# Optimization experiments

Measured on AMD Instinct MI355X. Metric: run time of the kernel, lower is better.

The kernel has to match this reference:

```python
import math
import jax, jax.numpy as jnp
import numpy as np

B, L, D, H = 2, 2048, 1024, 16
DH = D // H

def setup_inputs() -> dict:
    key = jax.random.key(0)
    ks = jax.random.split(key, 8)
    def xavier(k, fan_in, fan_out, shape):
        lim = math.sqrt(6.0 / (fan_in + fan_out))
        return jax.random.uniform(k, shape, jnp.float32, -lim, lim)
    x = jax.random.normal(ks[0], (B, L, D), jnp.float32)
    mask = jnp.ones((B, L), jnp.int32)
    # weights stored (in, out) so y = x @ W + b (equivalent to torch Linear)
    W_qkv = xavier(ks[1], D, 3 * D, (D, 3 * D))
    b_qkv = jnp.zeros((3 * D,), jnp.float32)
    W_out = xavier(ks[2], D, D, (D, D))
    b_out = jnp.zeros((D,), jnp.float32)
    W_phase = xavier(ks[3], D, H, (D, H))
    b_phase = jax.random.normal(ks[4], (H,), jnp.float32) * 0.02
    resonance_scale = jnp.float32(0.1)
    phase_scale = jnp.float32(1.0)
    return {"x": x, "mask": mask, "W_qkv": W_qkv, "b_qkv": b_qkv,
            "W_out": W_out, "b_out": b_out, "W_phase": W_phase,
            "b_phase": b_phase, "resonance_scale": resonance_scale,
            "phase_scale": phase_scale}

def reference(x, mask, W_qkv, b_qkv, W_out, b_out, W_phase, b_phase,
              resonance_scale, phase_scale):
    # qkv: (B,L,3D) -> (3,B,H,L,dh)
    qkv = (x @ W_qkv + b_qkv).reshape(B, L, 3, H, DH).transpose(2, 0, 3, 1, 4)
    q, k, v = qkv[0], qkv[1], qkv[2]
    scores = jnp.einsum('bhqd,bhkd->bhqk', q, k) / math.sqrt(DH)
    # per-token per-head phase (B,H,L)
    phase_val = jnp.tanh(phase_scale * (x @ W_phase + b_phase)).transpose(0, 2, 1)
    phase_diff = (phase_val[:, :, :, None] - phase_val[:, :, None, :]) ** 2
    scores = scores - resonance_scale * phase_diff
    # mask: (B,L) -> (B,1,1,L)
    m = mask[:, None, None, :]
    scores = jnp.where(m == 0, jnp.float32(-1e9), scores)
    attn = jax.nn.softmax(scores, axis=-1)
    out = jnp.einsum('bhqk,bhkd->bhqd', attn, v)  # (B,H,L,dh)
    out = out.transpose(0, 2, 1, 3).reshape(B, L, D)
    return out @ W_out + b_out
```

## Files before the change

kernel.cpp:

```cpp
#include <hip/hip_runtime.h>

typedef unsigned short u16;
typedef unsigned int u32;
typedef unsigned long long u64;
typedef __attribute__((ext_vector_type(2))) unsigned long long u64x2;
typedef __attribute__((ext_vector_type(4))) unsigned short u16x4;
typedef __attribute__((ext_vector_type(8))) __bf16 bf16x8;
typedef __attribute__((ext_vector_type(4))) float f32x4;
typedef __attribute__((ext_vector_type(2))) float f32x2;

#define DEV static __device__ __forceinline__
#define LOG2E 1.4426950408889634f

DEV u16 f2bf(float f) { __bf16 h = (__bf16)f; return __builtin_bit_cast(u16, h); }

#define BB   2
#define LLEN 2048
#define DDIM 1024
#define HH   16
#define DH   64
#define MTOT 4096
#define N3   3072

DEV void gl16(const void* g, void* l) {
  __builtin_amdgcn_global_load_lds(
      (const __attribute__((address_space(1))) void*)g,
      (__attribute__((address_space(3))) void*)l, 16, 0, 0);
}
DEV void gl4(const void* g, void* l) {
  __builtin_amdgcn_global_load_lds(
      (const __attribute__((address_space(1))) void*)g,
      (__attribute__((address_space(3))) void*)l, 4, 0, 0);
}

DEV void stage64(const u16* org, size_t gsb, u16* lds, int lane, int wid) {
#pragma unroll
  for (int j = 0; j < 2; j++) {
    int inst = wid * 2 + j;
    int r8 = lane >> 3;
    int row = inst * 8 + r8;
    int s = (r8 & 3) | ((inst & 1) << 2);
    const char* src = (const char*)org + (size_t)row * gsb +
                      (((lane & 7) ^ s) << 4);
    gl16(src, (char*)lds + inst * 1024);
  }
}
DEV bf16x8 read128s(const u16* tile, int row, int colb) {
  return *reinterpret_cast<const bf16x8*>(
      (const char*)tile + row * 128 +
      (colb ^ (((row & 3) | (((row >> 3) & 1) << 2)) << 4)));
}

DEV void stage128x32(const u16* org, size_t gsb, u16* lds, int lane, int wid) {
#pragma unroll
  for (int j = 0; j < 2; j++) {
    int inst = wid + j * 4;
    int r16 = lane >> 2;
    const char* src = (const char*)org + (size_t)(inst * 16 + r16) * gsb +
                      ((((lane & 3) ^ (r16 & 3))) << 4);
    gl16(src, (char*)lds + inst * 1024);
  }
}
DEV bf16x8 read64(const u16* tile, int row, int colb) {
  return *reinterpret_cast<const bf16x8*>(
      (const char*)tile + row * 64 + (colb ^ ((row & 3) << 4)));
}

__global__ __launch_bounds__(256) void k_transpose_w(const float* __restrict__ W,
                                                     u16* __restrict__ WT,
                                                     int K, int N) {
  __shared__ float s[32][33];
  int k0 = blockIdx.x * 32, n0 = blockIdx.y * 32;
  int tx = threadIdx.x & 31, ty = threadIdx.x >> 5;
#pragma unroll
  for (int i = 0; i < 4; i++)
    s[ty + i * 8][tx] = W[(k0 + ty + i * 8) * (size_t)N + n0 + tx];
  __syncthreads();
#pragma unroll
  for (int i = 0; i < 4; i++)
    WT[(size_t)(n0 + ty + i * 8) * K + k0 + tx] = f2bf(s[tx][ty + i * 8]);
}

__global__ __launch_bounds__(256) void k_phase(const float* __restrict__ x,
                                               const float* __restrict__ Wp,
                                               const float* __restrict__ bp,
                                               const float* __restrict__ pscale,
                                               const float* __restrict__ rscale,
                                               const int* __restrict__ mask,
                                               f32x2* __restrict__ ppk,
                                               u16* __restrict__ x_bf) {
  int m = blockIdx.x;
  int t = threadIdx.x;
  const float* xr = x + (size_t)m * DDIM;
  u16* xbr = x_bf + (size_t)m * DDIM;
  {
    f32x4 xv = *reinterpret_cast<const f32x4*>(xr + t * 4);
    u16x4 o;
    o.x = f2bf(xv.x); o.y = f2bf(xv.y); o.z = f2bf(xv.z); o.w = f2bf(xv.w);
    *reinterpret_cast<u16x4*>(xbr + t * 4) = o;
  }
  int h = t & 15, j = t >> 4;
  const float* wpb = Wp + h;
  float acc = 0.f;
#pragma unroll 4
  for (int kk4 = 0; kk4 < 16; kk4++) {
    int k0 = j * 64 + kk4 * 4;
    f32x4 xv = *reinterpret_cast<const f32x4*>(xr + k0);
    acc = fmaf(xv.x, wpb[(k0 + 0) * HH], acc);
    acc = fmaf(xv.y, wpb[(k0 + 1) * HH], acc);
    acc = fmaf(xv.z, wpb[(k0 + 2) * HH], acc);
    acc = fmaf(xv.w, wpb[(k0 + 3) * HH], acc);
  }
  __shared__ float s[16][17];
  s[j][h] = acc;
  __syncthreads();
  if (t < 16) {
    float sum = 0.f;
#pragma unroll
    for (int jj = 0; jj < 16; jj++) sum += s[jj][t];
    float v = tanhf((*pscale) * (sum + bp[t]));
    int b = m >> 11, l = m & (LLEN - 1);
    float kb = (mask[m] == 0) ? -1.0e9f : (-(*rscale) * LOG2E) * v * v;
    f32x2 o; o.x = v; o.y = kb;
    ppk[((size_t)(b * HH + t)) * LLEN + l] = o;
  }
}

template <bool BF16_OUT, bool QKV>
__global__ __launch_bounds__(256) void k_gemm(const u16* __restrict__ A,
                                              const u16* __restrict__ BT,
                                              const float* __restrict__ bias,
                                              void* __restrict__ C,
                                              u16* __restrict__ vT,
                                              int M, int N, int K) {
  __shared__ __attribute__((aligned(16))) u16 sS[4][128 * 32];
  int m0 = blockIdx.x * 128, n0 = blockIdx.y * 128;
  int t = threadIdx.x, lane = t & 63, wid = t >> 6;
  int wm = wid >> 1, wn = wid & 1;
  int lc = lane & 15, lg = lane >> 4;

  const u16* Ao = A + (size_t)m0 * K;
  const u16* Bo = BT + (size_t)n0 * K;

  f32x4 acc[4][4] = {};
  stage128x32(Ao, (size_t)K * 2, sS[0], lane, wid);
  stage128x32(Bo, (size_t)K * 2, sS[2], lane, wid);
  __syncthreads();
  int cur = 0;
  int NT = K >> 5;
  for (int kt = 0; kt < NT; kt++) {
    if (kt + 1 < NT) {
      stage128x32(Ao + (kt + 1) * 32, (size_t)K * 2, sS[cur ^ 1], lane, wid);
      stage128x32(Bo + (kt + 1) * 32, (size_t)K * 2, sS[2 + (cur ^ 1)], lane, wid);
    }
    bf16x8 af[4], bfr[4];
#pragma unroll
    for (int i = 0; i < 4; i++) af[i] = read64(sS[cur], wm * 64 + i * 16 + lc, lg * 16);
#pragma unroll
    for (int j = 0; j < 4; j++) bfr[j] = read64(sS[2 + cur], wn * 64 + j * 16 + lc, lg * 16);
    __builtin_amdgcn_s_setprio(1);
#pragma unroll
    for (int i = 0; i < 4; i++)
#pragma unroll
      for (int j = 0; j < 4; j++)
        acc[i][j] = __builtin_amdgcn_mfma_f32_16x16x32_bf16(af[i], bfr[j], acc[i][j], 0, 0, 0);
    __builtin_amdgcn_s_setprio(0);
    __syncthreads();
    cur ^= 1;
  }

  int rg = lane >> 4;
  if (QKV && n0 >= 2 * DDIM) {
    char* trS = (char*)&sS[0][0];
#pragma unroll
    for (int i = 0; i < 4; i++) {
      int rb = (wm * 64 + i * 16 + rg * 4) * 2;
#pragma unroll
      for (int j = 0; j < 4; j++) {
        int vc = wn * 64 + j * 16 + lc;
        float bv = bias[n0 + vc];
        u16 tmp[4];
#pragma unroll
        for (int r = 0; r < 4; r++) tmp[r] = f2bf(acc[i][j][r] + bv);
        *reinterpret_cast<u64*>(trS + vc * 256 + (rb ^ ((vc & 7) << 4))) =
            *reinterpret_cast<u64*>(tmp);
      }
    }
    __syncthreads();
    int bb = m0 >> 11, l0 = m0 & (LLEN - 1);
    int t7 = t & 7, tv = t >> 3;
#pragma unroll
    for (int p = 0; p < 4; p++) {
      int vc = p * 32 + tv;
      size_t vrow = ((size_t)bb * (HH * DH) + (n0 - 2 * DDIM) + vc) * LLEN + l0;
#pragma unroll
      for (int half = 0; half < 2; half++) {
        int rowbyte = t7 * 16 + half * 128;
        u64x2 v = *reinterpret_cast<const u64x2*>(
            trS + vc * 256 + (rowbyte ^ ((vc & 7) << 4)));
        *reinterpret_cast<u64x2*>(&vT[vrow + rowbyte / 2]) = v;
      }
    }
    return;
  }
#pragma unroll
  for (int i = 0; i < 4; i++) {
#pragma unroll
    for (int j = 0; j < 4; j++) {
      int col = n0 + wn * 64 + j * 16 + lc;
      float bv = bias[col];
#pragma unroll
      for (int r = 0; r < 4; r++) {
        int row = m0 + wm * 64 + i * 16 + rg * 4 + r;
        float v = acc[i][j][r] + bv;
        if (BF16_OUT)
          ((u16*)C)[(size_t)row * N + col] = f2bf(v);
        else
          ((float*)C)[(size_t)row * N + col] = v;
      }
    }
  }
}

__global__ __launch_bounds__(256, 4) void k_attn(const u16* __restrict__ qkv,
                                                 const u16* __restrict__ vT,
                                                 const f32x2* __restrict__ ppk,
                                                 const float* __restrict__ rscale_p,
                                                 u16* __restrict__ attn_out) {
  __shared__ __attribute__((aligned(16))) u16 kS[2][64 * 64];
  __shared__ __attribute__((aligned(16))) u16 vS[2][64 * 64];
  __shared__ __attribute__((aligned(16))) float ppS[2][128];

  int lin = blockIdx.y * 32 + blockIdx.x;
  int xcd = lin & 7, slot = lin >> 3;
  int bh = xcd * 4 + (slot >> 5);
  int q0 = (slot & 31) * 64;
  int b = bh >> 4, h = bh & 15;
  int t = threadIdx.x, lane = t & 63, wid = t >> 6;
  int qb = q0 + wid * 16;
  int lc = lane & 15, lg = lane >> 4;

  const float rs2 = (*rscale_p) * LOG2E;
  const float c1 = 0.125f * LOG2E;
  const f32x2* pprow = ppk + (size_t)bh * LLEN;
  const float* pprowf = (const float*)pprow;

  bf16x8 qf0, qf1;
  {
    const u16* qp = &qkv[(size_t)(b * LLEN + qb + lc) * N3 + h * DH + lg * 8];
    qf0 = *reinterpret_cast<const bf16x8*>(qp);
    qf1 = *reinterpret_cast<const bf16x8*>(qp + 32);
  }
  float wq = 2.f * rs2 * pprow[qb + lc].x;

  const u16* kg = qkv + (size_t)(b * LLEN) * N3 + DDIM + h * DH;
  const u16* vg = vT + (size_t)bh * DH * LLEN;

  stage64(kg, (size_t)N3 * 2, kS[0], lane, wid);
  stage64(vg, (size_t)LLEN * 2, vS[0], lane, wid);
  gl4(pprowf + lane, &ppS[0][0]);
  gl4(pprowf + 64 + lane, &ppS[0][64]);

  f32x4 o[4] = {};
  float mrow = -1e30f, lrow = 0.f;
  int arow = ((lc >> 2) << 3) | (lc & 3);

#define ATTN_STEP(KB, CUR)                                                     \
  do {                                                                         \
    if ((KB) + 64 < LLEN) {                                                    \
      stage64(kg + (size_t)((KB) + 64) * N3, (size_t)N3 * 2, kS[(CUR) ^ 1],    \
              lane, wid);                                                      \
      stage64(vg + (KB) + 64, (size_t)LLEN * 2, vS[(CUR) ^ 1], lane, wid);     \
      const float* pt_ = pprowf + (size_t)((KB) + 64) * 2;                     \
      gl4(pt_ + lane, &ppS[(CUR) ^ 1][0]);                                     \
      gl4(pt_ + 64 + lane, &ppS[(CUR) ^ 1][64]);                               \
      asm volatile("s_waitcnt vmcnt(6)" ::: "memory");                         \
    } else {                                                                   \
      asm volatile("s_waitcnt vmcnt(0)" ::: "memory");                         \
    }                                                                          \
    __builtin_amdgcn_s_barrier();                                              \
    f32x4 sv[4];                                                               \
    _Pragma("unroll") for (int blk = 0; blk < 4; blk++) {                      \
      int krow = arow + ((blk & 2) << 4) + ((blk & 1) << 2);                   \
      bf16x8 kf0 = read128s(kS[CUR], krow, lg * 16);                           \
      bf16x8 kf1 = read128s(kS[CUR], krow, 64 + lg * 16);                      \
      f32x4 z = {};                                                            \
      __builtin_amdgcn_s_setprio(1);                                           \
      z = __builtin_amdgcn_mfma_f32_16x16x32_bf16(kf0, qf0, z, 0, 0, 0);       \
      z = __builtin_amdgcn_mfma_f32_16x16x32_bf16(kf1, qf1, z, 0, 0, 0);       \
      __builtin_amdgcn_s_setprio(0);                                           \
      sv[blk] = z;                                                             \
    }                                                                          \
    {                                                                          \
      const float* pt_ = &ppS[CUR][0];                                         \
      _Pragma("unroll") for (int blk = 0; blk < 4; blk++) {                    \
        int off2 = (((blk & 2) << 4) + ((blk & 1) << 2) + lg * 8) * 2;         \
        f32x4 p0 = *reinterpret_cast<const f32x4*>(pt_ + off2);                \
        f32x4 p1 = *reinterpret_cast<const f32x4*>(pt_ + off2 + 4);            \
        sv[blk][0] = fmaf(sv[blk][0], c1, fmaf(wq, p0.x, p0.y));               \
        sv[blk][1] = fmaf(sv[blk][1], c1, fmaf(wq, p0.z, p0.w));               \
        sv[blk][2] = fmaf(sv[blk][2], c1, fmaf(wq, p1.x, p1.y));               \
        sv[blk][3] = fmaf(sv[blk][3], c1, fmaf(wq, p1.z, p1.w));               \
      }                                                                        \
    }                                                                          \
    float rm = sv[0][0];                                                       \
    _Pragma("unroll") for (int blk = 0; blk < 4; blk++)                        \
        _Pragma("unroll") for (int r = 0; r < 4; r++)                          \
            rm = fmaxf(rm, sv[blk][r]);                                        \
    rm = fmaxf(rm, __shfl_xor(rm, 16, 64));                                    \
    rm = fmaxf(rm, __shfl_xor(rm, 32, 64));                                    \
    if (!__all(rm <= mrow + 8.f)) {                                            \
      float mn = fmaxf(mrow, rm);                                              \
      float al = __builtin_amdgcn_exp2f(mrow - mn);                            \
      mrow = mn;                                                               \
      lrow *= al;                                                              \
      float ao0 = __shfl(al, lg * 4 + 0, 16);                                  \
      float ao1 = __shfl(al, lg * 4 + 1, 16);                                  \
      float ao2 = __shfl(al, lg * 4 + 2, 16);                                  \
      float ao3 = __shfl(al, lg * 4 + 3, 16);                                  \
      _Pragma("unroll") for (int d = 0; d < 4; d++) {                          \
        o[d][0] *= ao0; o[d][1] *= ao1; o[d][2] *= ao2; o[d][3] *= ao3;        \
      }                                                                        \
    }                                                                          \
    float ssum = 0.f;                                                          \
    _Pragma("unroll") for (int blk = 0; blk < 4; blk++)                        \
        _Pragma("unroll") for (int r = 0; r < 4; r++) {                        \
      float p = __builtin_amdgcn_exp2f(sv[blk][r] - mrow);                     \
      sv[blk][r] = p;                                                          \
      ssum += p;                                                               \
    }                                                                          \
    ssum += __shfl_xor(ssum, 16, 64);                                          \
    ssum += __shfl_xor(ssum, 32, 64);                                          \
    lrow += ssum;                                                              \
    bf16x8 pa0, pa1;                                                           \
    _Pragma("unroll") for (int r = 0; r < 4; r++) {                            \
      pa0[r] = (__bf16)sv[0][r];                                               \
      pa0[4 + r] = (__bf16)sv[1][r];                                           \
      pa1[r] = (__bf16)sv[2][r];                                               \
      pa1[4 + r] = (__bf16)sv[3][r];                                           \
    }                                                                          \
    _Pragma("unroll") for (int d = 0; d < 4; d++) {                            \
      bf16x8 vb0 = read128s(vS[CUR], d * 16 + lc, lg * 16);                    \
      bf16x8 vb1 = read128s(vS[CUR], d * 16 + lc, 64 + lg * 16);               \
      __builtin_amdgcn_s_setprio(1);                                           \
      o[d] = __builtin_amdgcn_mfma_f32_16x16x32_bf16(pa0, vb0, o[d], 0, 0, 0); \
      o[d] = __builtin_amdgcn_mfma_f32_16x16x32_bf16(pa1, vb1, o[d], 0, 0, 0); \
      __builtin_amdgcn_s_setprio(0);                                           \
    }                                                                          \
    __builtin_amdgcn_s_barrier();                                              \
  } while (0)

  for (int kt = 0; kt < LLEN / 64; kt += 2) {
    ATTN_STEP(kt * 64, 0);
    ATTN_STEP(kt * 64 + 64, 1);
  }
#undef ATTN_STEP

  float linv = 1.0f / lrow;
  float li0 = __shfl(linv, lg * 4 + 0, 16);
  float li1 = __shfl(linv, lg * 4 + 1, 16);
  float li2 = __shfl(linv, lg * 4 + 2, 16);
  float li3 = __shfl(linv, lg * 4 + 3, 16);
#pragma unroll
  for (int d = 0; d < 4; d++) {
    int col = h * DH + d * 16 + lc;
    size_t base = (size_t)(b * LLEN + qb + lg * 4) * DDIM + col;
    attn_out[base] = f2bf(o[d][0] * li0);
    attn_out[base + DDIM] = f2bf(o[d][1] * li1);
    attn_out[base + 2 * DDIM] = f2bf(o[d][2] * li2);
    attn_out[base + 3 * DDIM] = f2bf(o[d][3] * li3);
  }
}

extern "C" void kernel_launch(void* const* d_in, const int* in_sizes, int n_in,
                              void* d_out, int out_size, void* d_ws, size_t ws_size,
                              hipStream_t stream) {
  const float* x       = (const float*)d_in[0];
  const int*   mask    = (const int*)d_in[1];
  const float* W_qkv   = (const float*)d_in[2];
  const float* b_qkv   = (const float*)d_in[3];
  const float* W_out   = (const float*)d_in[4];
  const float* b_out   = (const float*)d_in[5];
  const float* W_phase = (const float*)d_in[6];
  const float* b_phase = (const float*)d_in[7];
  const float* rscale  = (const float*)d_in[8];
  const float* pscale  = (const float*)d_in[9];
  float* out = (float*)d_out;

  char* ws = (char*)d_ws;
  u16* x_bf     = (u16*)(ws + 0);
  u16* wt_qkv   = (u16*)(ws + 8388608);
  u16* wt_out   = (u16*)(ws + 14680064);
  u16* qkv      = (u16*)(ws + 16777216);
  u16* vT       = (u16*)(ws + 41943040);
  u16* attn_out = (u16*)(ws + 50331648);
  f32x2* ppk    = (f32x2*)(ws + 58720256);

  k_transpose_w<<<dim3(DDIM / 32, N3 / 32), 256, 0, stream>>>(W_qkv, wt_qkv, DDIM, N3);
  k_transpose_w<<<dim3(DDIM / 32, DDIM / 32), 256, 0, stream>>>(W_out, wt_out, DDIM, DDIM);
  k_phase<<<MTOT, 256, 0, stream>>>(x, W_phase, b_phase, pscale, rscale, mask, ppk, x_bf);
  k_gemm<true, true><<<dim3(MTOT / 128, N3 / 128), 256, 0, stream>>>(
      x_bf, wt_qkv, b_qkv, qkv, vT, MTOT, N3, DDIM);
  k_attn<<<dim3(LLEN / 64, BB * HH), 256, 0, stream>>>(
      qkv, vT, ppk, rscale, attn_out);
  k_gemm<false, false><<<dim3(MTOT / 128, DDIM / 128), 256, 0, stream>>>(
      attn_out, wt_out, b_out, out, nullptr, MTOT, DDIM, DDIM);
}
```

Measured before the change: 232.9 us.

## Merge weight transposes, tile out-proj GEMM narrower, compute softmax rowsum via MFMA

The two weight-transpose launches become a single kernel that dispatches on blockIdx.y. The GEMM is templated on the N tile width so the output projection uses 64-wide tiles, doubling its grid from 256 to 512 blocks for better CU fill. In attention, the per-step exp-sum and cross-lane shuffle reduction are replaced by two extra MFMAs against a ones vector that accumulate the row sum. The row-max reduction is also rebalanced into a shallower tree. These add MFMA work per step and reduce reuse in the output GEMM.

```diff
diff --git a/kernel.cpp b/kernel.cpp
--- a/kernel.cpp
+++ b/kernel.cpp
@@ -51,9 +51,10 @@
       (colb ^ (((row & 3) | (((row >> 3) & 1) << 2)) << 4)));
 }
 
-DEV void stage128x32(const u16* org, size_t gsb, u16* lds, int lane, int wid) {
-#pragma unroll
-  for (int j = 0; j < 2; j++) {
+template <int ROWS>
+DEV void stageR32(const u16* org, size_t gsb, u16* lds, int lane, int wid) {
+#pragma unroll
+  for (int j = 0; j < ROWS / 64; j++) {
     int inst = wid + j * 4;
     int r16 = lane >> 2;
     const char* src = (const char*)org + (size_t)(inst * 16 + r16) * gsb +
@@ -66,11 +67,18 @@
       (const char*)tile + row * 64 + (colb ^ ((row & 3) << 4)));
 }
 
-__global__ __launch_bounds__(256) void k_transpose_w(const float* __restrict__ W,
-                                                     u16* __restrict__ WT,
-                                                     int K, int N) {
+__global__ __launch_bounds__(256) void k_transpose_w2(const float* __restrict__ Wq,
+                                                      const float* __restrict__ Wo,
+                                                      u16* __restrict__ WTq,
+                                                      u16* __restrict__ WTo) {
   __shared__ float s[32][33];
-  int k0 = blockIdx.x * 32, n0 = blockIdx.y * 32;
+  int y = blockIdx.y;
+  const float* W;
+  u16* WT;
+  int N, n0;
+  if (y < 96) { W = Wq; WT = WTq; N = N3; n0 = y * 32; }
+  else        { W = Wo; WT = WTo; N = DDIM; n0 = (y - 96) * 32; }
+  int k0 = blockIdx.x * 32;
   int tx = threadIdx.x & 31, ty = threadIdx.x >> 5;
 #pragma unroll
   for (int i = 0; i < 4; i++)
@@ -78,7 +86,7 @@
   __syncthreads();
 #pragma unroll
   for (int i = 0; i < 4; i++)
-    WT[(size_t)(n0 + ty + i * 8) * K + k0 + tx] = f2bf(s[tx][ty + i * 8]);
+    WT[(size_t)(n0 + ty + i * 8) * DDIM + k0 + tx] = f2bf(s[tx][ty + i * 8]);
 }
 
 __global__ __launch_bounds__(256) void k_phase(const float* __restrict__ x,
@@ -126,15 +134,17 @@
   }
 }
 
-template <bool BF16_OUT, bool QKV>
+template <bool BF16_OUT, bool QKV, int BN>
 __global__ __launch_bounds__(256) void k_gemm(const u16* __restrict__ A,
                                               const u16* __restrict__ BT,
                                               const float* __restrict__ bias,
                                               void* __restrict__ C,
                                               u16* __restrict__ vT,
                                               int M, int N, int K) {
-  __shared__ __attribute__((aligned(16))) u16 sS[4][128 * 32];
-  int m0 = blockIdx.x * 128, n0 = blockIdx.y * 128;
+  __shared__ __attribute__((aligned(16))) u16 sA[2][128 * 32];
+  __shared__ __attribute__((aligned(16))) u16 sB[2][BN * 32];
+  constexpr int NW = BN / 32;
+  int m0 = blockIdx.x * 128, n0 = blockIdx.y * BN;
   int t = threadIdx.x, lane = t & 63, wid = t >> 6;
   int wm = wid >> 1, wn = wid & 1;
   int lc = lane & 15, lg = lane >> 4;
@@ -142,27 +152,27 @@
   const u16* Ao = A + (size_t)m0 * K;
   const u16* Bo = BT + (size_t)n0 * K;
 
-  f32x4 acc[4][4] = {};
-  stage128x32(Ao, (size_t)K * 2, sS[0], lane, wid);
-  stage128x32(Bo, (size_t)K * 2, sS[2], lane, wid);
+  f32x4 acc[4][NW] = {};
+  stageR32<128>(Ao, (size_t)K * 2, sA[0], lane, wid);
+  stageR32<BN>(Bo, (size_t)K * 2, sB[0], lane, wid);
   __syncthreads();
   int cur = 0;
   int NT = K >> 5;
   for (int kt = 0; kt < NT; kt++) {
     if (kt + 1 < NT) {
-      stage128x32(Ao + (kt + 1) * 32, (size_t)K * 2, sS[cur ^ 1], lane, wid);
-      stage128x32(Bo + (kt + 1) * 32, (size_t)K * 2, sS[2 + (cur ^ 1)], lane, wid);
+      stageR32<128>(Ao + (kt + 1) * 32, (size_t)K * 2, sA[cur ^ 1], lane, wid);
+      stageR32<BN>(Bo + (kt + 1) * 32, (size_t)K * 2, sB[cur ^ 1], lane, wid);
     }
-    bf16x8 af[4], bfr[4];
-#pragma unroll
-    for (int i = 0; i < 4; i++) af[i] = read64(sS[cur], wm * 64 + i * 16 + lc, lg * 16);
-#pragma unroll
-    for (int j = 0; j < 4; j++) bfr[j] = read64(sS[2 + cur], wn * 64 + j * 16 + lc, lg * 16);
+    bf16x8 af[4], bfr[NW];
+#pragma unroll
+    for (int i = 0; i < 4; i++) af[i] = read64(sA[cur], wm * 64 + i * 16 + lc, lg * 16);
+#pragma unroll
+    for (int j = 0; j < NW; j++) bfr[j] = read64(sB[cur], wn * (BN / 2) + j * 16 + lc, lg * 16);
     __builtin_amdgcn_s_setprio(1);
 #pragma unroll
     for (int i = 0; i < 4; i++)
 #pragma unroll
-      for (int j = 0; j < 4; j++)
+      for (int j = 0; j < NW; j++)
         acc[i][j] = __builtin_amdgcn_mfma_f32_16x16x32_bf16(af[i], bfr[j], acc[i][j], 0, 0, 0);
     __builtin_amdgcn_s_setprio(0);
     __syncthreads();
@@ -170,44 +180,49 @@
   }
 
   int rg = lane >> 4;
-  if (QKV && n0 >= 2 * DDIM) {
-    char* trS = (char*)&sS[0][0];
-#pragma unroll
-    for (int i = 0; i < 4; i++) {
-      int rb = (wm * 64 + i * 16 + rg * 4) * 2;
-#pragma unroll
-      for (int j = 0; j < 4; j++) {
-        int vc = wn * 64 + j * 16 + lc;
-        float bv = bias[n0 + vc];
-        u16 tmp[4];
-#pragma unroll
-        for (int r = 0; r < 4; r++) tmp[r] = f2bf(acc[i][j][r] + bv);
-        *reinterpret_cast<u64*>(trS + vc * 256 + (rb ^ ((vc & 7) << 4))) =
-            *reinterpret_cast<u64*>(tmp);
+  if constexpr (QKV) {
+    if (n0 >= 2 * DDIM) {
+      char* halfW = wn ? (char*)&sB[0][0] : (char*)&sA[0][0];
+#pragma unroll
+      for (int i = 0; i < 4; i++) {
+        int rb = (wm * 64 + i * 16 + rg * 4) * 2;
+#pragma unroll
+        for (int j = 0; j < NW; j++) {
+          int vcl = j * 16 + lc;
+          int vc = wn * 64 + vcl;
+          float bv = bias[n0 + vc];
+          u16 tmp[4];
+#pragma unroll
+          for (int r = 0; r < 4; r++) tmp[r] = f2bf(acc[i][j][r] + bv);
+          *reinterpret_cast<u64*>(halfW + vcl * 256 + (rb ^ ((vc & 7) << 4))) =
+              *reinterpret_cast<u64*>(tmp);
+        }
       }
+      __syncthreads();
+      int bb = m0 >> 11, l0 = m0 & (LLEN - 1);
+      int t7 = t & 7, tv = t >> 3;
+#pragma unroll
+      for (int p = 0; p < 4; p++) {
+        int vc = p * 32 + tv;
+        char* halfR = (vc & 64) ? (char*)&sB[0][0] : (char*)&sA[0][0];
+        int vcl = vc & 63;
+        size_t vrow = ((size_t)bb * (HH * DH) + (n0 - 2 * DDIM) + vc) * LLEN + l0;
+#pragma unroll
+        for (int half = 0; half < 2; half++) {
+          int rowbyte = t7 * 16 + half * 128;
+          u64x2 v = *reinterpret_cast<const u64x2*>(
+              halfR + vcl * 256 + (rowbyte ^ ((vc & 7) << 4)));
+          *reinterpret_cast<u64x2*>(&vT[vrow + rowbyte / 2]) = v;
+        }
+      }
+      return;
     }
-    __syncthreads();
-    int bb = m0 >> 11, l0 = m0 & (LLEN - 1);
-    int t7 = t & 7, tv = t >> 3;
-#pragma unroll
-    for (int p = 0; p < 4; p++) {
-      int vc = p * 32 + tv;
-      size_t vrow = ((size_t)bb * (HH * DH) + (n0 - 2 * DDIM) + vc) * LLEN + l0;
-#pragma unroll
-      for (int half = 0; half < 2; half++) {
-        int rowbyte = t7 * 16 + half * 128;
-        u64x2 v = *reinterpret_cast<const u64x2*>(
-            trS + vc * 256 + (rowbyte ^ ((vc & 7) << 4)));
-        *reinterpret_cast<u64x2*>(&vT[vrow + rowbyte / 2]) = v;
-      }
-    }
-    return;
   }
 #pragma unroll
   for (int i = 0; i < 4; i++) {
 #pragma unroll
-    for (int j = 0; j < 4; j++) {
-      int col = n0 + wn * 64 + j * 16 + lc;
+    for (int j = 0; j < NW; j++) {
+      int col = n0 + wn * (BN / 2) + j * 16 + lc;
       float bv = bias[col];
 #pragma unroll
       for (int r = 0; r < 4; r++) {
@@ -245,6 +260,10 @@
   const f32x2* pprow = ppk + (size_t)bh * LLEN;
   const float* pprowf = (const float*)pprow;
 
+  bf16x8 ONES;
+#pragma unroll
+  for (int j = 0; j < 8; j++) ONES[j] = (__bf16)1.0f;
+
   bf16x8 qf0, qf1;
   {
     const u16* qp = &qkv[(size_t)(b * LLEN + qb + lc) * N3 + h * DH + lg * 8];
@@ -262,7 +281,8 @@
   gl4(pprowf + 64 + lane, &ppS[0][64]);
 
   f32x4 o[4] = {};
-  float mrow = -1e30f, lrow = 0.f;
+  f32x4 lrow4 = {};
+  float mrow = -1e30f;
   int arow = ((lc >> 2) << 3) | (lc & 3);
 
 #define ATTN_STEP(KB, CUR)                                                     \
@@ -303,17 +323,21 @@
         sv[blk][3] = fmaf(sv[blk][3], c1, fmaf(wq, p1.z, p1.w));               \
       }                                                                        \
     }                                                                          \
-    float rm = sv[0][0];                                                       \
-    _Pragma("unroll") for (int blk = 0; blk < 4; blk++)                        \
-        _Pragma("unroll") for (int r = 0; r < 4; r++)                          \
-            rm = fmaxf(rm, sv[blk][r]);                                        \
+                                    \
+    float a_ = fmaxf(fmaxf(sv[0][0], sv[0][1]), sv[0][2]);                     \
+    float b_ = fmaxf(fmaxf(sv[0][3], sv[1][0]), sv[1][1]);                     \
+    float c_ = fmaxf(fmaxf(sv[1][2], sv[1][3]), sv[2][0]);                     \
+    float d_ = fmaxf(fmaxf(sv[2][1], sv[2][2]), sv[2][3]);                     \
+    float e_ = fmaxf(fmaxf(sv[3][0], sv[3][1]), sv[3][2]);                     \
+    float rm = fmaxf(fmaxf(a_, b_), c_);                                       \
+    float rm2 = fmaxf(fmaxf(d_, e_), sv[3][3]);                                \
+    rm = fmaxf(rm, rm2);                                                       \
     rm = fmaxf(rm, __shfl_xor(rm, 16, 64));                                    \
     rm = fmaxf(rm, __shfl_xor(rm, 32, 64));                                    \
     if (!__all(rm <= mrow + 8.f)) {                                            \
       float mn = fmaxf(mrow, rm);                                              \
       float al = __builtin_amdgcn_exp2f(mrow - mn);                            \
       mrow = mn;                                                               \
-      lrow *= al;                                                              \
       float ao0 = __shfl(al, lg * 4 + 0, 16);                                  \
       float ao1 = __shfl(al, lg * 4 + 1, 16);                                  \
       float ao2 = __shfl(al, lg * 4 + 2, 16);                                  \
@@ -321,17 +345,11 @@
       _Pragma("unroll") for (int d = 0; d < 4; d++) {                          \
         o[d][0] *= ao0; o[d][1] *= ao1; o[d][2] *= ao2; o[d][3] *= ao3;        \
       }                                                                        \
-    }                                                                          \
-    float ssum = 0.f;                                                          \
+      lrow4[0] *= ao0; lrow4[1] *= ao1; lrow4[2] *= ao2; lrow4[3] *= ao3;      \
+    }                                                                          \
     _Pragma("unroll") for (int blk = 0; blk < 4; blk++)                        \
-        _Pragma("unroll") for (int r = 0; r < 4; r++) {                        \
-      float p = __builtin_amdgcn_exp2f(sv[blk][r] - mrow);                     \
-      sv[blk][r] = p;                                                          \
-      ssum += p;                                                               \
-    }                                                                          \
-    ssum += __shfl_xor(ssum, 16, 64);                                          \
-    ssum += __shfl_xor(ssum, 32, 64);                                          \
-    lrow += ssum;                                                              \
+        _Pragma("unroll") for (int r = 0; r < 4; r++)                          \
+            sv[blk][r] = __builtin_amdgcn_exp2f(sv[blk][r] - mrow);            \
     bf16x8 pa0, pa1;                                                           \
     _Pragma("unroll") for (int r = 0; r < 4; r++) {                            \
       pa0[r] = (__bf16)sv[0][r];                                               \
@@ -347,6 +365,9 @@
       o[d] = __builtin_amdgcn_mfma_f32_16x16x32_bf16(pa1, vb1, o[d], 0, 0, 0); \
       __builtin_amdgcn_s_setprio(0);                                           \
     }                                                                          \
+                                       \
+    lrow4 = __builtin_amdgcn_mfma_f32_16x16x32_bf16(pa0, ONES, lrow4, 0, 0, 0);\
+    lrow4 = __builtin_amdgcn_mfma_f32_16x16x32_bf16(pa1, ONES, lrow4, 0, 0, 0);\
     __builtin_amdgcn_s_barrier();                                              \
   } while (0)
 
@@ -356,11 +377,10 @@
   }
 #undef ATTN_STEP
 
-  float linv = 1.0f / lrow;
-  float li0 = __shfl(linv, lg * 4 + 0, 16);
-  float li1 = __shfl(linv, lg * 4 + 1, 16);
-  float li2 = __shfl(linv, lg * 4 + 2, 16);
-  float li3 = __shfl(linv, lg * 4 + 3, 16);
+  float li0 = 1.0f / lrow4[0];
+  float li1 = 1.0f / lrow4[1];
+  float li2 = 1.0f / lrow4[2];
+  float li3 = 1.0f / lrow4[3];
 #pragma unroll
   for (int d = 0; d < 4; d++) {
     int col = h * DH + d * 16 + lc;
@@ -396,13 +416,12 @@
   u16* attn_out = (u16*)(ws + 50331648);
   f32x2* ppk    = (f32x2*)(ws + 58720256);
 
-  k_transpose_w<<<dim3(DDIM / 32, N3 / 32), 256, 0, stream>>>(W_qkv, wt_qkv, DDIM, N3);
-  k_transpose_w<<<dim3(DDIM / 32, DDIM / 32), 256, 0, stream>>>(W_out, wt_out, DDIM, DDIM);
+  k_transpose_w2<<<dim3(DDIM / 32, 128), 256, 0, stream>>>(W_qkv, W_out, wt_qkv, wt_out);
   k_phase<<<MTOT, 256, 0, stream>>>(x, W_phase, b_phase, pscale, rscale, mask, ppk, x_bf);
-  k_gemm<true, true><<<dim3(MTOT / 128, N3 / 128), 256, 0, stream>>>(
+  k_gemm<true, true, 128><<<dim3(MTOT / 128, N3 / 128), 256, 0, stream>>>(
       x_bf, wt_qkv, b_qkv, qkv, vT, MTOT, N3, DDIM);
   k_attn<<<dim3(LLEN / 64, BB * HH), 256, 0, stream>>>(
       qkv, vT, ppk, rscale, attn_out);
-  k_gemm<false, false><<<dim3(MTOT / 128, DDIM / 128), 256, 0, stream>>>(
+  k_gemm<false, false, 64><<<dim3(MTOT / 128, DDIM / 64), 256, 0, stream>>>(
       attn_out, wt_out, b_out, out, nullptr, MTOT, DDIM, DDIM);
 }
```

New measurement: 231.8 us. Within noise of the previous version (-0.4%).
